# Performance work log

Hardware: AMD Instinct MI355X
Metric: run time of the kernel (lower is better)

## Reference

```python
import jax, jax.numpy as jnp
import numpy as np

B, N, T, F_IN = 4, 1024, 16, 32
H1, H2 = 128, 128
LH = H2 // 2          # LSTM hidden = 64
MLP_H = H2 // 4       # 32
NEG = -9e15
ALPHA = 0.2           # LeakyReLU slope


def _xavier(k, shape):
    lim = float(np.sqrt(6.0 / (shape[0] + shape[1])))
    return jax.random.uniform(k, shape, jnp.float32, -lim, lim)


def _unif(k, shape, s):
    return jax.random.uniform(k, shape, jnp.float32, -s, s)


def setup_inputs() -> dict:
    key = jax.random.key(0)
    ks = jax.random.split(key, 16)
    x = jax.random.normal(ks[0], (B, N, T, F_IN), dtype=jnp.float32)
    adj = jax.random.randint(ks[1], (B, N, N), 0, 2, dtype=jnp.int32)
    # GAT layer 1 & 2
    W1 = _xavier(ks[2], (F_IN, H1)); a1 = _xavier(ks[3], (2 * H1, 1))
    W2 = _xavier(ks[4], (H1, H2));   a2 = _xavier(ks[5], (2 * H2, 1))
    # LSTM (torch gate order i,f,g,o)
    s = 1.0 / np.sqrt(LH)
    W_ih = _unif(ks[6], (4 * LH, H2), s)
    W_hh = _unif(ks[7], (4 * LH, LH), s)
    b_ih = _unif(ks[8], (4 * LH,), s)
    b_hh = _unif(ks[9], (4 * LH,), s)
    # Output MLP: 64 -> 32 -> 1
    s1 = 1.0 / np.sqrt(LH)
    Wo1 = _unif(ks[10], (LH, MLP_H), s1); bo1 = _unif(ks[11], (MLP_H,), s1)
    s2 = 1.0 / np.sqrt(MLP_H)
    Wo2 = _unif(ks[12], (MLP_H, 1), s2);  bo2 = _unif(ks[13], (1,), s2)
    return {"x": x, "adj": adj, "W1": W1, "a1": a1, "W2": W2, "a2": a2,
            "W_ih": W_ih, "W_hh": W_hh, "b_ih": b_ih, "b_hh": b_hh,
            "Wo1": Wo1, "bo1": bo1, "Wo2": Wo2, "bo2": bo2}


def _gat(h, mask, W, a):
    # h: (B,N,Fin) -> (B,N,Fout). Decompose cat([Wh_i,Wh_j]) @ a into two rank-1 scores.
    Wh = h @ W                             # (B,N,Fout)
    Fo = W.shape[1]
    s_src = Wh @ a[:Fo, 0]                 # (B,N)
    s_dst = Wh @ a[Fo:, 0]                 # (B,N)
    e = jax.nn.leaky_relu(s_src[:, :, None] + s_dst[:, None, :], ALPHA)  # (B,N,N)
    att = jnp.where(mask, e, NEG)
    att = jax.nn.softmax(att, axis=-1)
    return jax.nn.elu(att @ Wh)            # GAT layer's own ELU (concat=True)


def reference(x, adj, W1, a1, W2, a2, W_ih, W_hh, b_ih, b_hh, Wo1, bo1, Wo2, bo2):
    mask = adj > 0                         # (B,N,N)

    def per_t(ht):                         # ht: (B,N,F_IN)
        h = jax.nn.elu(_gat(ht, mask, W1, a1))   # outer F.elu as in GNNModel.forward
        h = jax.nn.elu(_gat(h, mask, W2, a2))
        return h

    g = jax.vmap(per_t, in_axes=2, out_axes=2)(x)   # (B,N,T,H2)
    seq = g.reshape(B * N, T, H2)

    def step(carry, xt):
        h, c = carry
        gates = xt @ W_ih.T + b_ih + h @ W_hh.T + b_hh
        i, f, gg, o = jnp.split(gates, 4, axis=-1)
        c = jax.nn.sigmoid(f) * c + jax.nn.sigmoid(i) * jnp.tanh(gg)
        h = jax.nn.sigmoid(o) * jnp.tanh(c)
        return (h, c), None

    init = (jnp.zeros((B * N, LH), x.dtype), jnp.zeros((B * N, LH), x.dtype))
    (hT, _), _ = jax.lax.scan(step, init, jnp.swapaxes(seq, 0, 1))  # scan over T

    out = jax.nn.relu(hT @ Wo1 + bo1) @ Wo2 + bo2   # (B*N, 1)
    return out.reshape(B, N, 1)
```

## Files before the change

### kernel.cpp

```cpp
#include <hip/hip_runtime.h>
#include <hip/hip_bf16.h>
#include <math.h>

#define BB 4
#define NN 1024
#define TT 16
#define FIN 32
#define HH 128
#define LH 64
#define MLPH 32

typedef __attribute__((ext_vector_type(8))) short short8;
typedef __attribute__((ext_vector_type(4))) float f32x4;
typedef unsigned short u16;
typedef unsigned int u32;

union AFu { u32 u[4]; short8 s; };

__device__ __forceinline__ u16 f2b(float f) {
    union { float f; u32 u; } v; v.f = f;
    u32 u = v.u;
    return (u16)((u + 0x7FFFu + ((u >> 16) & 1u)) >> 16);
}
__device__ __forceinline__ float b2f(u16 h) {
    union { u32 u; float f; } v; v.u = ((u32)h) << 16;
    return v.f;
}
__device__ __forceinline__ float frcp(float x) {
    float r; asm("v_rcp_f32 %0, %1" : "=v"(r) : "v"(x)); return r;
}
__device__ __forceinline__ float fsig(float x) {
    return frcp(1.f + __expf(-x));
}
__device__ __forceinline__ float ftanh(float x) {
    return __builtin_fmaf(2.f, frcp(1.f + __expf(-2.f * x)), -1.f);
}
__device__ __forceinline__ void gload_lds16(const void* g, void* l) {
    __builtin_amdgcn_global_load_lds((const __attribute__((address_space(1))) unsigned int*)g,
                                     (__attribute__((address_space(3))) unsigned int*)l, 16, 0, 0);
}

__global__ __launch_bounds__(256) void k_pre(const float* __restrict__ W1, const float* __restrict__ W2,
                      const float* __restrict__ W_ih, const float* __restrict__ W_hh,
                      const float* __restrict__ b_ih, const float* __restrict__ b_hh,
                      u16* W1T, u16* W2T, u16* WihB, u16* WhhB, float* bsum) {
    int gi = blockIdx.x * 256 + threadIdx.x;
    for (int i = gi; i < 128 * 32; i += 16384) { int c = i >> 5, k = i & 31; W1T[i] = f2b(W1[k * 128 + c]); }
    for (int i = gi; i < 128 * 128; i += 16384) { int c = i >> 7, k = i & 127; W2T[i] = f2b(W2[k * 128 + c]); }
    for (int i = gi; i < 256 * 128; i += 16384) WihB[i] = f2b(W_ih[i]);
    for (int i = gi; i < 256 * 64; i += 16384) WhhB[i] = f2b(W_hh[i]);
    if (gi < 256) bsum[gi] = b_ih[gi] + b_hh[gi];
}

__global__ __launch_bounds__(256) void k_mask(const int* __restrict__ adj, u32* __restrict__ bmT) {
    int gw = (blockIdx.x * 256 + threadIdx.x) >> 6;
    int lane = threadIdx.x & 63;
    int base = gw << 4;
#pragma unroll 4
    for (int it = 0; it < 16; ++it) {
        int u = base + it;
        unsigned long long m = __ballot(adj[((size_t)u << 6) + lane] > 0);
        if (lane == 0) {
            int g = u & 15;
            int bi = u >> 4;
            int b = bi >> 10, i = bi & 1023;
            bmT[(((b << 5) + 2 * g) << 10) + i]     = (u32)m;
            bmT[(((b << 5) + 2 * g + 1) << 10) + i] = (u32)(m >> 32);
        }
    }
}


__global__ __launch_bounds__(256) void k_projA(const float* __restrict__ x, const u16* __restrict__ W1T,
                                               const float* __restrict__ a1,
                                               u16* __restrict__ WhT, float* __restrict__ ssrc,
                                               float* __restrict__ sdst) {
    __shared__ float tile[64][132];
    __shared__ float sA[256];
    int bt = blockIdx.x >> 4, i0 = (blockIdx.x & 15) << 6;
    int b = bt >> 4, t = bt & 15;
    int tid = threadIdx.x, w = tid >> 6, l = tid & 63;
    int lr = l & 15, lg = l >> 4;
    sA[tid] = a1[tid];
    int i = i0 + 16 * w + lr;
    const float* xp = x + ((size_t)((b << 10) + i) * TT + t) * FIN + 8 * lg;
    float4 x0 = *(const float4*)xp;
    float4 x1 = *(const float4*)(xp + 4);
    short8 af;
    af[0] = (short)f2b(x0.x); af[1] = (short)f2b(x0.y); af[2] = (short)f2b(x0.z); af[3] = (short)f2b(x0.w);
    af[4] = (short)f2b(x1.x); af[5] = (short)f2b(x1.y); af[6] = (short)f2b(x1.z); af[7] = (short)f2b(x1.w);
    f32x4 zz = {0.f, 0.f, 0.f, 0.f};
#pragma unroll
    for (int tc = 0; tc < 8; ++tc) {
        short8 bf = *(const short8*)(W1T + ((16 * tc + lr) << 5) + 8 * lg);
        f32x4 d = __builtin_amdgcn_mfma_f32_16x16x32_bf16(af, bf, zz, 0, 0, 0);
#pragma unroll
        for (int r = 0; r < 4; ++r) tile[16 * w + 4 * lg + r][16 * tc + lr] = d[r];
    }
    __syncthreads();
    if (tid < 128) {
        int r = tid & 63;
        const float* av = sA + ((tid < 64) ? 0 : 128);
        float s = 0.f;
#pragma unroll 4
        for (int c = 0; c < 128; ++c) s += tile[r][c] * av[c];
        ((tid < 64) ? ssrc : sdst)[(bt << 10) + i0 + r] = s;
    }
    {
        int c = tid & 127, hh2 = tid >> 7;
        u16 tmp[32];
#pragma unroll
        for (int j = 0; j < 32; ++j) tmp[j] = f2b(tile[32 * hh2 + j][c]);
        int tc = c >> 4, lr2 = c & 15;
        u16* dst = WhT + (size_t)bt * 131072 + ((i0 >> 5) + hh2) * 4096 + tc * 512 + lr2 * 8;
#pragma unroll
        for (int lg2 = 0; lg2 < 4; ++lg2) *(short8*)(dst + lg2 * 128) = *(const short8*)(tmp + 8 * lg2);
    }
}

__global__ __launch_bounds__(256) void k_projB(const u16* __restrict__ h1, const u16* __restrict__ W2T,
                                               const float* __restrict__ a2,
                                               u16* __restrict__ WhT, float* __restrict__ ssrc,
                                               float* __restrict__ sdst) {
    __shared__ float tile[64][132];
    __shared__ float sA[256];
    int bt = blockIdx.x >> 4, i0 = (blockIdx.x & 15) << 6;
    int tid = threadIdx.x, w = tid >> 6, l = tid & 63;
    int lr = l & 15, lg = l >> 4;
    sA[tid] = a2[tid];
    const u16* ap = h1 + (size_t)bt * 131072 + ((i0 >> 4) + w) * 2048 + l * 8;
    f32x4 acc[8];
#pragma unroll
    for (int tc = 0; tc < 8; ++tc) acc[tc] = (f32x4){0.f, 0.f, 0.f, 0.f};
#pragma unroll
    for (int ch = 0; ch < 4; ++ch) {
        short8 af = *(const short8*)(ap + ch * 512);
#pragma unroll
        for (int tc = 0; tc < 8; ++tc) {
            short8 bf = *(const short8*)(W2T + ((16 * tc + lr) << 7) + 32 * ch + 8 * lg);
            acc[tc] = __builtin_amdgcn_mfma_f32_16x16x32_bf16(af, bf, acc[tc], 0, 0, 0);
        }
    }
#pragma unroll
    for (int tc = 0; tc < 8; ++tc)
#pragma unroll
        for (int r = 0; r < 4; ++r) tile[16 * w + 4 * lg + r][16 * tc + lr] = acc[tc][r];
    __syncthreads();
    if (tid < 128) {
        int r = tid & 63;
        const float* av = sA + ((tid < 64) ? 0 : 128);
        float s = 0.f;
#pragma unroll 4
        for (int c = 0; c < 128; ++c) s += tile[r][c] * av[c];
        ((tid < 64) ? ssrc : sdst)[(bt << 10) + i0 + r] = s;
    }
    {
        int c = tid & 127, hh2 = tid >> 7;
        u16 tmp[32];
#pragma unroll
        for (int j = 0; j < 32; ++j) tmp[j] = f2b(tile[32 * hh2 + j][c]);
        int tc = c >> 4, lr2 = c & 15;
        u16* dst = WhT + (size_t)bt * 131072 + ((i0 >> 5) + hh2) * 4096 + tc * 512 + lr2 * 8;
#pragma unroll
        for (int lg2 = 0; lg2 < 4; ++lg2) *(short8*)(dst + lg2 * 128) = *(const short8*)(tmp + 8 * lg2);
    }
}

template <bool GX>
__global__ __launch_bounds__(512, 2) void k_attn(const u16* __restrict__ WhT, const float* __restrict__ ssrc,
                                                 const float* __restrict__ sdst, const u32* __restrict__ bmT,
                                                 u16* __restrict__ hout, const u16* __restrict__ WihB,
                                                 const float* __restrict__ bsum, u16* __restrict__ Gx) {
    __shared__ __align__(16) u16 Bbuf[2][8192];
    __shared__ __align__(16) float Ej[1024];
    __shared__ __align__(16) float Fj[1024];
    int bt = blockIdx.x >> 2, i0b = (blockIdx.x & 3) << 8;
    int b = bt >> 4;
    int tid = threadIdx.x, wv = tid >> 6, l = tid & 63;
    int lr = l & 15, lg = l >> 4;
    const u16* wbase = WhT + (size_t)bt * 131072;

    gload_lds16(wbase + (wv << 10) + l * 8,       &Bbuf[0][(wv << 10)]);
    gload_lds16(wbase + (wv << 10) + 512 + l * 8, &Bbuf[0][(wv << 10) + 512]);

    for (int k = tid; k < 1024; k += 512) {
        float sdv = sdst[(bt << 10) + k];
        Ej[k] = __expf(sdv);
        Fj[k] = __expf(0.2f * sdv);
    }
    int rb = i0b + (wv << 5);
    const u32* mbase = bmT + ((size_t)b << 15);
    u32 mw0 = mbase[rb + lr];
    u32 mw1 = mbase[rb + 16 + lr];
    u32 mw2 = mbase[1024 + rb + lr];
    u32 mw3 = mbase[1024 + rb + 16 + lr];
    float si0 = ssrc[(bt << 10) + rb + lr];
    float si1 = ssrc[(bt << 10) + rb + 16 + lr];
    float Ei0 = __expf(si0), Fi0 = __expf(0.2f * si0);
    float Ei1 = __expf(si1), Fi1 = __expf(0.2f * si1);
    f32x4 acc[2][8];
#pragma unroll
    for (int rt = 0; rt < 2; ++rt)
#pragma unroll
        for (int tc = 0; tc < 8; ++tc) acc[rt][tc] = (f32x4){0.f, 0.f, 0.f, 0.f};
    f32x4 accd[2];
    accd[0] = (f32x4){0.f, 0.f, 0.f, 0.f};
    accd[1] = (f32x4){0.f, 0.f, 0.f, 0.f};
    short8 bone;
#pragma unroll
    for (int e = 0; e < 8; ++e) bone[e] = (short)0x3F80;
    __syncthreads();

#define PHALF(AF, EI, FI, WW)                                                        \
    {                                                                                \
        u32 byt = ((WW) >> (lg << 3)) & 0xFFu;                                       \
        float pA[8] = {fmaxf((EI) * e0.x, (FI) * f0.x), fmaxf((EI) * e0.y, (FI) * f0.y), \
                       fmaxf((EI) * e0.z, (FI) * f0.z), fmaxf((EI) * e0.w, (FI) * f0.w), \
                       fmaxf((EI) * e1.x, (FI) * f1.x), fmaxf((EI) * e1.y, (FI) * f1.y), \
                       fmaxf((EI) * e1.z, (FI) * f1.z), fmaxf((EI) * e1.w, (FI) * f1.w)}; \
        _Pragma("unroll")                                                            \
        for (int q = 0; q < 4; ++q) {                                                \
            u32 m0 = (u32)(-(int)((byt >> (2 * q)) & 1u));                           \
            u32 m1 = (u32)(-(int)((byt >> (2 * q + 1)) & 1u));                       \
            float p0 = __uint_as_float(__float_as_uint(pA[2 * q]) & m0);             \
            float p1 = __uint_as_float(__float_as_uint(pA[2 * q + 1]) & m1);         \
            asm("v_cvt_pk_bf16_f32 %0, %1, %2" : "=v"(AF.u[q]) : "v"(p0), "v"(p1));  \
        }                                                                            \
    }

#define COMPUTE(JC, CUR, JCL, W0, W1)                                                \
    {                                                                                \
        short8 bfr[8];                                                               \
        _Pragma("unroll")                                                            \
        for (int tc = 0; tc < 8; ++tc)                                               \
            bfr[tc] = *(const short8*)(&Bbuf[CUR][(JCL) * 4096 + tc * 512 + l * 8]); \
        const float* ejp = Ej + ((JC) << 5) + (lg << 3);                             \
        const float* fjp = Fj + ((JC) << 5) + (lg << 3);                             \
        float4 e0 = *(const float4*)ejp, e1 = *(const float4*)(ejp + 4);             \
        float4 f0 = *(const float4*)fjp, f1 = *(const float4*)(fjp + 4);             \
        AFu af0, af1;                                                                \
        PHALF(af0, Ei0, Fi0, W0)                                                     \
        PHALF(af1, Ei1, Fi1, W1)                                                     \
        _Pragma("unroll")                                                            \
        for (int tc = 0; tc < 8; ++tc) {                                             \
            acc[0][tc] = __builtin_amdgcn_mfma_f32_16x16x32_bf16(af0.s, bfr[tc], acc[0][tc], 0, 0, 0); \
            acc[1][tc] = __builtin_amdgcn_mfma_f32_16x16x32_bf16(af1.s, bfr[tc], acc[1][tc], 0, 0, 0); \
        }                                                                            \
        accd[0] = __builtin_amdgcn_mfma_f32_16x16x32_bf16(af0.s, bone, accd[0], 0, 0, 0); \
        accd[1] = __builtin_amdgcn_mfma_f32_16x16x32_bf16(af1.s, bone, accd[1], 0, 0, 0); \
    }

    for (int c = 0; c < 16; ++c) {
        int cur = c & 1;
        if (c < 15) {
            gload_lds16(wbase + (c + 1) * 8192 + (wv << 10) + l * 8,       &Bbuf[cur ^ 1][(wv << 10)]);
            gload_lds16(wbase + (c + 1) * 8192 + (wv << 10) + 512 + l * 8, &Bbuf[cur ^ 1][(wv << 10) + 512]);
        }
        u32 nw0 = 0, nw1 = 0, nw2 = 0, nw3 = 0;
        if (c < 15) {
            const u32* mp = mbase + ((2 * c + 2) << 10);
            nw0 = mp[rb + lr];        nw1 = mp[rb + 16 + lr];
            nw2 = mp[1024 + rb + lr]; nw3 = mp[1024 + rb + 16 + lr];
        }
        COMPUTE(2 * c,     cur, 0, mw0, mw1)
        COMPUTE(2 * c + 1, cur, 1, mw2, mw3)
        mw0 = nw0; mw1 = nw1; mw2 = nw2; mw3 = nw3;
        __syncthreads();
    }
#undef PHALF
#undef COMPUTE

    char* hb = (char*)(&Bbuf[0][0]) + (wv << 12);
    int t = bt & 15;
    for (int rt = 0; rt < 2; ++rt) {
        float inv[4];
#pragma unroll
        for (int r = 0; r < 4; ++r) inv[r] = 1.f / accd[rt][r];
#pragma unroll
        for (int tc = 0; tc < 8; ++tc)
#pragma unroll
            for (int r = 0; r < 4; ++r) {
                float v = acc[rt][tc][r] * inv[r];
                v = v > 0.f ? v : (__expf(v) - 1.f);
                v = v > 0.f ? v : (__expf(v) - 1.f);
                int row = (lg << 2) + r;
                int col = (tc << 4) + lr;
                *(u16*)(hb + (row << 8) + ((col << 1) ^ ((row & 7) << 4))) = f2b(v);
            }
        asm volatile("s_waitcnt lgkmcnt(0)" ::: "memory");
        __builtin_amdgcn_sched_barrier(0);
        if (!GX) {
            int rtile = (rb >> 4) + rt;
            u16* dstb = hout + (size_t)bt * 131072;
#pragma unroll
            for (int ch = 0; ch < 4; ++ch) {
                int colb = (ch << 5) + (lg << 3);
                short8 v = *(const short8*)(hb + (lr << 8) + ((colb << 1) ^ ((lr & 7) << 4)));
                *(short8*)(dstb + (size_t)rtile * 2048 + ch * 512 + l * 8) = v;
            }
        } else {
            int node = i0b + (wv << 5) + (rt << 4);
            int grp = (b << 6) + (node >> 4);
            u16* gdst = Gx + (size_t)t * 1048576 + (size_t)grp * 4096 + l * 8;
#pragma unroll
            for (int half = 0; half < 2; ++half) {
                f32x4 accg[8];
#pragma unroll
                for (int tq = 0; tq < 8; ++tq) accg[tq] = (f32x4){0.f, 0.f, 0.f, 0.f};
#pragma unroll
                for (int ch = 0; ch < 4; ++ch) {
                    short8 af2 = *(const short8*)(hb + (lr << 8) + (((ch << 6) + (lg << 4)) ^ ((lr & 7) << 4)));
#pragma unroll
                    for (int tq = 0; tq < 8; ++tq) {
                        int tc = (half << 3) + tq;
                        short8 bf = *(const short8*)(WihB + ((16 * tc + lr) << 7) + (ch << 5) + 8 * lg);
                        accg[tq] = __builtin_amdgcn_mfma_f32_16x16x32_bf16(af2, bf, accg[tq], 0, 0, 0);
                    }
                }
#pragma unroll
                for (int qq = 0; qq < 4; ++qq) {
                    int tc0 = (half << 3) + 2 * qq;
                    short8 v;
#pragma unroll
                    for (int r = 0; r < 4; ++r) {
                        v[r]     = (short)f2b(accg[2 * qq][r]     + bsum[(tc0 << 4) + lr]);
                        v[4 + r] = (short)f2b(accg[2 * qq + 1][r] + bsum[((tc0 + 1) << 4) + lr]);
                    }
                    *(short8*)(gdst + ((half << 2) + qq) * 512) = v;
                }
            }
        }
        if (rt == 0) { asm volatile("s_waitcnt lgkmcnt(0)" ::: "memory"); }
    }
}

__global__ __launch_bounds__(64, 1) void k_lstm(const u16* __restrict__ Gx, const u16* __restrict__ WhhB,
                                                const float* __restrict__ Wo1, const float* __restrict__ bo1,
                                                const float* __restrict__ Wo2, const float* __restrict__ bo2,
                                                float* __restrict__ out) {
    __shared__ u16 hls[16 * 72];
    __shared__ float hf[16 * 65];
    __shared__ float wo1[64 * 32];
    __shared__ float wo2[32];
    int grp = blockIdx.x;
    int m0 = grp << 4;
    int l = threadIdx.x, lr = l & 15, lg = l >> 4;
    for (int k = l; k < 64 * 32; k += 64) wo1[k] = Wo1[k];
    if (l < 32) wo2[l] = Wo2[l];
    for (int k = l; k < 16 * 72; k += 64) hls[k] = 0;
    short8 bh[16][2];
#pragma unroll
    for (int tc = 0; tc < 16; ++tc)
#pragma unroll
        for (int ch = 0; ch < 2; ++ch)
            bh[tc][ch] = *(const short8*)(WhhB + ((16 * tc + lr) << 6) + 32 * ch + 8 * lg);
    float cst[4][4], hreg[4][4];
#pragma unroll
    for (int r = 0; r < 4; ++r)
#pragma unroll
        for (int q = 0; q < 4; ++q) cst[r][q] = 0.f;
    const u16* gp = Gx + ((size_t)grp << 12) + l * 8;
    short8 gx0[8], gx1[8];
#pragma unroll
    for (int q = 0; q < 8; ++q) gx0[q] = *(const short8*)(gp + q * 512);
    __syncthreads();
#pragma unroll
    for (int t = 0; t < TT; ++t) {
        if (t < 15) {
#pragma unroll
            for (int q = 0; q < 8; ++q) {
                short8 v = *(const short8*)(gp + (size_t)(t + 1) * 1048576 + q * 512);
                if (t & 1) gx0[q] = v; else gx1[q] = v;
            }
        }
        f32x4 acc[16];
#pragma unroll
        for (int q = 0; q < 8; ++q) {
            short8 v = (t & 1) ? gx1[q] : gx0[q];
#pragma unroll
            for (int r = 0; r < 4; ++r) {
                acc[2 * q][r]     = b2f((u16)v[r]);
                acc[2 * q + 1][r] = b2f((u16)v[4 + r]);
            }
        }
#pragma unroll
        for (int ch = 0; ch < 2; ++ch) {
            short8 af = *(const short8*)(hls + lr * 72 + 32 * ch + 8 * lg);
#pragma unroll
            for (int tc = 0; tc < 16; ++tc)
                acc[tc] = __builtin_amdgcn_mfma_f32_16x16x32_bf16(af, bh[tc][ch], acc[tc], 0, 0, 0);
        }
#pragma unroll
        for (int r = 0; r < 4; ++r)
#pragma unroll
            for (int q = 0; q < 4; ++q) {
                float iv = fsig(acc[q][r]);
                float fv = fsig(acc[q + 4][r]);
                float gv = ftanh(acc[q + 8][r]);
                float ov = fsig(acc[q + 12][r]);
                float cn = __builtin_fmaf(fv, cst[r][q], iv * gv);
                cst[r][q] = cn;
                hreg[r][q] = ov * ftanh(cn);
            }
        __syncthreads();
#pragma unroll
        for (int r = 0; r < 4; ++r)
#pragma unroll
            for (int q = 0; q < 4; ++q)
                hls[(4 * lg + r) * 72 + 16 * q + lr] = f2b(hreg[r][q]);
        __syncthreads();
    }
#pragma unroll
    for (int r = 0; r < 4; ++r)
#pragma unroll
        for (int q = 0; q < 4; ++q)
            hf[(4 * lg + r) * 65 + 16 * q + lr] = hreg[r][q];
    __syncthreads();
    {
        int r = l & 15, p = l >> 4;
        float hid[8];
#pragma unroll
        for (int q = 0; q < 8; ++q) hid[q] = bo1[8 * p + q];
        for (int j = 0; j < 64; ++j) {
            float hv = hf[r * 65 + j];
#pragma unroll
            for (int q = 0; q < 8; ++q) hid[q] += hv * wo1[j * 32 + 8 * p + q];
        }
        float po = 0.f;
#pragma unroll
        for (int q = 0; q < 8; ++q) po += fmaxf(hid[q], 0.f) * wo2[8 * p + q];
        po += __shfl_xor(po, 16);
        po += __shfl_xor(po, 32);
        if (p == 0) out[m0 + r] = po + bo2[0];
    }
}

extern "C" void kernel_launch(void* const* d_in, const int* in_sizes, int n_in,
                              void* d_out, int out_size, void* d_ws, size_t ws_size,
                              hipStream_t stream) {
    const float* x    = (const float*)d_in[0];
    const int*   adj  = (const int*)d_in[1];
    const float* W1   = (const float*)d_in[2];
    const float* a1   = (const float*)d_in[3];
    const float* W2   = (const float*)d_in[4];
    const float* a2   = (const float*)d_in[5];
    const float* W_ih = (const float*)d_in[6];
    const float* W_hh = (const float*)d_in[7];
    const float* b_ih = (const float*)d_in[8];
    const float* b_hh = (const float*)d_in[9];
    const float* Wo1  = (const float*)d_in[10];
    const float* bo1  = (const float*)d_in[11];
    const float* Wo2  = (const float*)d_in[12];
    const float* bo2  = (const float*)d_in[13];
    float* out = (float*)d_out;

    char* w = (char*)d_ws;
    const size_t SLOT = (size_t)8388608 * sizeof(u16);
    u16* A  = (u16*)w;
    u16* Bf = (u16*)(w + SLOT);
    u16* C  = (u16*)(w + 2 * SLOT);
    char* sm = w + 3 * SLOT;
    float* s1s = (float*)sm;
    float* s1d = s1s + 65536;
    float* s2s = s1d + 65536;
    float* s2d = s2s + 65536;
    u32* BM  = (u32*)(s2d + 65536);
    u16* W1T = (u16*)(BM + 131072);
    u16* W2T = W1T + 4096;
    u16* WihB = W2T + 16384;
    u16* WhhB = WihB + 32768;
    float* BS = (float*)(WhhB + 16384);
    u16* Gx = Bf;

    k_pre<<<64, 256, 0, stream>>>(W1, W2, W_ih, W_hh, b_ih, b_hh, W1T, W2T, WihB, WhhB, BS);
    k_mask<<<1024, 256, 0, stream>>>(adj, BM);
    k_projA<<<1024, 256, 0, stream>>>(x, W1T, a1, A, s1s, s1d);
    k_attn<false><<<256, 512, 0, stream>>>(A, s1s, s1d, BM, Bf, nullptr, nullptr, nullptr);
    k_projB<<<1024, 256, 0, stream>>>(Bf, W2T, a2, C, s2s, s2d);
    k_attn<true><<<256, 512, 0, stream>>>(C, s2s, s2d, BM, nullptr, WihB, BS, Gx);
    k_lstm<<<256, 64, 0, stream>>>(Gx, WhhB, Wo1, bo1, Wo2, bo2, out);
}
```

Measured before the change: 183.5 us.

## Split LSTM gate tiles across four waves and restructure attention epilogue

The LSTM kernel goes from one wave per 16-row group to four waves, each owning a 16-column slice of every gate. That cuts the serial MFMA chain and gate math per wave by four, but each step now needs a block-wide barrier to exchange h through LDS. The attention epilogue's two-iteration loop is unrolled into macros, dropping the conditional wait so the compiler can schedule straight-line code. This is meant to shorten the latency-bound recurrent loop, which runs on only 256 single-wave blocks.

```diff
diff --git a/kernel.cpp b/kernel.cpp
--- a/kernel.cpp
+++ b/kernel.cpp
@@ -272,152 +272,161 @@
 
     char* hb = (char*)(&Bbuf[0][0]) + (wv << 12);
     int t = bt & 15;
-    for (int rt = 0; rt < 2; ++rt) {
-        float inv[4];
-#pragma unroll
-        for (int r = 0; r < 4; ++r) inv[r] = 1.f / accd[rt][r];
-#pragma unroll
-        for (int tc = 0; tc < 8; ++tc)
-#pragma unroll
-            for (int r = 0; r < 4; ++r) {
-                float v = acc[rt][tc][r] * inv[r];
-                v = v > 0.f ? v : (__expf(v) - 1.f);
-                v = v > 0.f ? v : (__expf(v) - 1.f);
-                int row = (lg << 2) + r;
-                int col = (tc << 4) + lr;
-                *(u16*)(hb + (row << 8) + ((col << 1) ^ ((row & 7) << 4))) = f2b(v);
-            }
-        asm volatile("s_waitcnt lgkmcnt(0)" ::: "memory");
-        __builtin_amdgcn_sched_barrier(0);
-        if (!GX) {
-            int rtile = (rb >> 4) + rt;
-            u16* dstb = hout + (size_t)bt * 131072;
-#pragma unroll
-            for (int ch = 0; ch < 4; ++ch) {
-                int colb = (ch << 5) + (lg << 3);
-                short8 v = *(const short8*)(hb + (lr << 8) + ((colb << 1) ^ ((lr & 7) << 4)));
-                *(short8*)(dstb + (size_t)rtile * 2048 + ch * 512 + l * 8) = v;
-            }
-        } else {
-            int node = i0b + (wv << 5) + (rt << 4);
-            int grp = (b << 6) + (node >> 4);
-            u16* gdst = Gx + (size_t)t * 1048576 + (size_t)grp * 4096 + l * 8;
-#pragma unroll
-            for (int half = 0; half < 2; ++half) {
-                f32x4 accg[8];
-#pragma unroll
-                for (int tq = 0; tq < 8; ++tq) accg[tq] = (f32x4){0.f, 0.f, 0.f, 0.f};
-#pragma unroll
-                for (int ch = 0; ch < 4; ++ch) {
-                    short8 af2 = *(const short8*)(hb + (lr << 8) + (((ch << 6) + (lg << 4)) ^ ((lr & 7) << 4)));
-#pragma unroll
-                    for (int tq = 0; tq < 8; ++tq) {
-                        int tc = (half << 3) + tq;
-                        short8 bf = *(const short8*)(WihB + ((16 * tc + lr) << 7) + (ch << 5) + 8 * lg);
-                        accg[tq] = __builtin_amdgcn_mfma_f32_16x16x32_bf16(af2, bf, accg[tq], 0, 0, 0);
-                    }
-                }
-#pragma unroll
-                for (int qq = 0; qq < 4; ++qq) {
-                    int tc0 = (half << 3) + 2 * qq;
-                    short8 v;
-#pragma unroll
-                    for (int r = 0; r < 4; ++r) {
-                        v[r]     = (short)f2b(accg[2 * qq][r]     + bsum[(tc0 << 4) + lr]);
-                        v[4 + r] = (short)f2b(accg[2 * qq + 1][r] + bsum[((tc0 + 1) << 4) + lr]);
-                    }
-                    *(short8*)(gdst + ((half << 2) + qq) * 512) = v;
-                }
-            }
-        }
-        if (rt == 0) { asm volatile("s_waitcnt lgkmcnt(0)" ::: "memory"); }
-    }
-}
-
-__global__ __launch_bounds__(64, 1) void k_lstm(const u16* __restrict__ Gx, const u16* __restrict__ WhhB,
-                                                const float* __restrict__ Wo1, const float* __restrict__ bo1,
-                                                const float* __restrict__ Wo2, const float* __restrict__ bo2,
-                                                float* __restrict__ out) {
+
+#define EPI_STORE(RT)                                                                 \
+    {                                                                                 \
+        float inv[4];                                                                 \
+        _Pragma("unroll")                                                             \
+        for (int r = 0; r < 4; ++r) inv[r] = 1.f / accd[RT][r];                       \
+        _Pragma("unroll")                                                             \
+        for (int tc = 0; tc < 8; ++tc)                                                \
+            _Pragma("unroll")                                                         \
+            for (int r = 0; r < 4; ++r) {                                             \
+                float v = acc[RT][tc][r] * inv[r];                                    \
+                v = v > 0.f ? v : (__expf(v) - 1.f);                                  \
+                v = v > 0.f ? v : (__expf(v) - 1.f);                                  \
+                int row = (lg << 2) + r;                                              \
+                int col = (tc << 4) + lr;                                             \
+                *(u16*)(hb + (row << 8) + ((col << 1) ^ ((row & 7) << 4))) = f2b(v);  \
+            }                                                                         \
+        asm volatile("s_waitcnt lgkmcnt(0)" ::: "memory");                            \
+        __builtin_amdgcn_sched_barrier(0);                                            \
+    }
+
+#define EPI_OUT_H(RT)                                                                 \
+    {                                                                                 \
+        int rtile = (rb >> 4) + (RT);                                                 \
+        u16* dstb = hout + (size_t)bt * 131072;                                       \
+        _Pragma("unroll")                                                             \
+        for (int ch = 0; ch < 4; ++ch) {                                              \
+            int colb = (ch << 5) + (lg << 3);                                         \
+            short8 v = *(const short8*)(hb + (lr << 8) + ((colb << 1) ^ ((lr & 7) << 4))); \
+            *(short8*)(dstb + (size_t)rtile * 2048 + ch * 512 + l * 8) = v;           \
+        }                                                                             \
+    }
+
+#define EPI_OUT_GX(RT)                                                                \
+    {                                                                                 \
+        int node = i0b + (wv << 5) + ((RT) << 4);                                     \
+        int grpx = (b << 6) + (node >> 4);                                            \
+        u16* gdst = Gx + (size_t)t * 1048576 + (size_t)grpx * 4096 + l * 8;           \
+        _Pragma("unroll")                                                             \
+        for (int half = 0; half < 2; ++half) {                                        \
+            f32x4 accg[8];                                                            \
+            _Pragma("unroll")                                                         \
+            for (int tq = 0; tq < 8; ++tq) accg[tq] = (f32x4){0.f, 0.f, 0.f, 0.f};    \
+            _Pragma("unroll")                                                         \
+            for (int ch = 0; ch < 4; ++ch) {                                          \
+                short8 af2 = *(const short8*)(hb + (lr << 8) + (((ch << 6) + (lg << 4)) ^ ((lr & 7) << 4))); \
+                _Pragma("unroll")                                                     \
+                for (int tq = 0; tq < 8; ++tq) {                                      \
+                    int tc = (half << 3) + tq;                                        \
+                    short8 bf = *(const short8*)(WihB + ((16 * tc + lr) << 7) + (ch << 5) + 8 * lg); \
+                    accg[tq] = __builtin_amdgcn_mfma_f32_16x16x32_bf16(af2, bf, accg[tq], 0, 0, 0); \
+                }                                                                     \
+            }                                                                         \
+            _Pragma("unroll")                                                         \
+            for (int qq = 0; qq < 4; ++qq) {                                          \
+                int tc0 = (half << 3) + 2 * qq;                                       \
+                short8 v;                                                             \
+                _Pragma("unroll")                                                     \
+                for (int r = 0; r < 4; ++r) {                                         \
+                    v[r]     = (short)f2b(accg[2 * qq][r]     + bsum[(tc0 << 4) + lr]); \
+                    v[4 + r] = (short)f2b(accg[2 * qq + 1][r] + bsum[((tc0 + 1) << 4) + lr]); \
+                }                                                                     \
+                *(short8*)(gdst + ((half << 2) + qq) * 512) = v;                      \
+            }                                                                         \
+        }                                                                             \
+    }
+
+    EPI_STORE(0)
+    if (!GX) { EPI_OUT_H(0) } else { EPI_OUT_GX(0) }
+    asm volatile("s_waitcnt lgkmcnt(0)" ::: "memory");
+    __builtin_amdgcn_sched_barrier(0);
+    EPI_STORE(1)
+    if (!GX) { EPI_OUT_H(1) } else { EPI_OUT_GX(1) }
+
+#undef EPI_STORE
+#undef EPI_OUT_H
+#undef EPI_OUT_GX
+}
+
+__global__ __launch_bounds__(256, 1) void k_lstm(const u16* __restrict__ Gx, const u16* __restrict__ WhhB,
+                                                 const float* __restrict__ Wo1, const float* __restrict__ bo1,
+                                                 const float* __restrict__ Wo2, const float* __restrict__ bo2,
+                                                 float* __restrict__ out) {
     __shared__ u16 hls[16 * 72];
     __shared__ float hf[16 * 65];
     __shared__ float wo1[64 * 32];
     __shared__ float wo2[32];
     int grp = blockIdx.x;
     int m0 = grp << 4;
-    int l = threadIdx.x, lr = l & 15, lg = l >> 4;
-    for (int k = l; k < 64 * 32; k += 64) wo1[k] = Wo1[k];
-    if (l < 32) wo2[l] = Wo2[l];
-    for (int k = l; k < 16 * 72; k += 64) hls[k] = 0;
-    short8 bh[16][2];
-#pragma unroll
-    for (int tc = 0; tc < 16; ++tc)
+    int tid = threadIdx.x, wv = tid >> 6, l = tid & 63;
+    int lr = l & 15, lg = l >> 4;
+    for (int k = tid; k < 64 * 32; k += 256) wo1[k] = Wo1[k];
+    if (tid < 32) wo2[tid] = Wo2[tid];
+    for (int k = tid; k < 16 * 72; k += 256) hls[k] = 0;
+    short8 bh[4][2];
+#pragma unroll
+    for (int tq = 0; tq < 4; ++tq)
 #pragma unroll
         for (int ch = 0; ch < 2; ++ch)
-            bh[tc][ch] = *(const short8*)(WhhB + ((16 * tc + lr) << 6) + 32 * ch + 8 * lg);
-    float cst[4][4], hreg[4][4];
-#pragma unroll
-    for (int r = 0; r < 4; ++r)
-#pragma unroll
-        for (int q = 0; q < 4; ++q) cst[r][q] = 0.f;
-    const u16* gp = Gx + ((size_t)grp << 12) + l * 8;
-    short8 gx0[8], gx1[8];
-#pragma unroll
-    for (int q = 0; q < 8; ++q) gx0[q] = *(const short8*)(gp + q * 512);
+            bh[tq][ch] = *(const short8*)(WhhB + ((16 * (wv + 4 * tq) + lr) << 6) + 32 * ch + 8 * lg);
+    float cst[4], hreg[4];
+#pragma unroll
+    for (int r = 0; r < 4; ++r) { cst[r] = 0.f; hreg[r] = 0.f; }
+    int sub = wv & 1;
+    const u16* gp = Gx + ((size_t)grp << 12) + ((size_t)(wv >> 1) << 9) + l * 8;
+    short8 gx0[4], gx1[4];
+#pragma unroll
+    for (int tq = 0; tq < 4; ++tq) gx0[tq] = *(const short8*)(gp + tq * 1024);
     __syncthreads();
 #pragma unroll
     for (int t = 0; t < TT; ++t) {
         if (t < 15) {
 #pragma unroll
-            for (int q = 0; q < 8; ++q) {
-                short8 v = *(const short8*)(gp + (size_t)(t + 1) * 1048576 + q * 512);
-                if (t & 1) gx0[q] = v; else gx1[q] = v;
+            for (int tq = 0; tq < 4; ++tq) {
+                short8 v = *(const short8*)(gp + (size_t)(t + 1) * 1048576 + tq * 1024);
+                if (t & 1) gx0[tq] = v; else gx1[tq] = v;
             }
         }
-        f32x4 acc[16];
-#pragma unroll
-        for (int q = 0; q < 8; ++q) {
-            short8 v = (t & 1) ? gx1[q] : gx0[q];
-#pragma unroll
-            for (int r = 0; r < 4; ++r) {
-                acc[2 * q][r]     = b2f((u16)v[r]);
-                acc[2 * q + 1][r] = b2f((u16)v[4 + r]);
-            }
+        f32x4 acc[4];
+#pragma unroll
+        for (int tq = 0; tq < 4; ++tq) {
+            short8 v = (t & 1) ? gx1[tq] : gx0[tq];
+#pragma unroll
+            for (int r = 0; r < 4; ++r)
+                acc[tq][r] = b2f((u16)v[(sub << 2) + r]);
         }
 #pragma unroll
         for (int ch = 0; ch < 2; ++ch) {
             short8 af = *(const short8*)(hls + lr * 72 + 32 * ch + 8 * lg);
 #pragma unroll
-            for (int tc = 0; tc < 16; ++tc)
-                acc[tc] = __builtin_amdgcn_mfma_f32_16x16x32_bf16(af, bh[tc][ch], acc[tc], 0, 0, 0);
-        }
+            for (int tq = 0; tq < 4; ++tq)
+                acc[tq] = __builtin_amdgcn_mfma_f32_16x16x32_bf16(af, bh[tq][ch], acc[tq], 0, 0, 0);
+        }
+#pragma unroll
+        for (int r = 0; r < 4; ++r) {
+            float iv = fsig(acc[0][r]);
+            float fv = fsig(acc[1][r]);
+            float gv = ftanh(acc[2][r]);
+            float ov = fsig(acc[3][r]);
+            float cn = __builtin_fmaf(fv, cst[r], iv * gv);
+            cst[r] = cn;
+            hreg[r] = ov * ftanh(cn);
+        }
+        __syncthreads();
 #pragma unroll
         for (int r = 0; r < 4; ++r)
-#pragma unroll
-            for (int q = 0; q < 4; ++q) {
-                float iv = fsig(acc[q][r]);
-                float fv = fsig(acc[q + 4][r]);
-                float gv = ftanh(acc[q + 8][r]);
-                float ov = fsig(acc[q + 12][r]);
-                float cn = __builtin_fmaf(fv, cst[r][q], iv * gv);
-                cst[r][q] = cn;
-                hreg[r][q] = ov * ftanh(cn);
-            }
+            hls[(4 * lg + r) * 72 + 16 * wv + lr] = f2b(hreg[r]);
         __syncthreads();
-#pragma unroll
-        for (int r = 0; r < 4; ++r)
-#pragma unroll
-            for (int q = 0; q < 4; ++q)
-                hls[(4 * lg + r) * 72 + 16 * q + lr] = f2b(hreg[r][q]);
-        __syncthreads();
     }
 #pragma unroll
     for (int r = 0; r < 4; ++r)
-#pragma unroll
-        for (int q = 0; q < 4; ++q)
-            hf[(4 * lg + r) * 65 + 16 * q + lr] = hreg[r][q];
+        hf[(4 * lg + r) * 65 + 16 * wv + lr] = hreg[r];
     __syncthreads();
-    {
-        int r = l & 15, p = l >> 4;
+    if (wv == 0) {
+        int r = lr, p = lg;
         float hid[8];
 #pragma unroll
         for (int q = 0; q < 8; ++q) hid[q] = bo1[8 * p + q];
@@ -478,5 +487,5 @@
     k_attn<false><<<256, 512, 0, stream>>>(A, s1s, s1d, BM, Bf, nullptr, nullptr, nullptr);
     k_projB<<<1024, 256, 0, stream>>>(Bf, W2T, a2, C, s2s, s2d);
     k_attn<true><<<256, 512, 0, stream>>>(C, s2s, s2d, BM, nullptr, WihB, BS, Gx);
-    k_lstm<<<256, 64, 0, stream>>>(Gx, WhhB, Wo1, bo1, Wo2, bo2, out);
-}
+    k_lstm<<<256, 256, 0, stream>>>(Gx, WhhB, Wo1, bo1, Wo2, bo2, out);
+}
```

Result: faster. 169.1 us (-7.8%).
